# Kernel tuning notes

Hardware: AMD Instinct MI355X
Metric: run time of the kernel (lower is better)

The kernel has to match this reference:

```python
import jax, jax.numpy as jnp
import numpy as np

B = 8192
D = 626
TEMP = 0.25
EPS = 1e-8


def setup_inputs() -> dict:
    key = jax.random.key(0)
    k1, k2 = jax.random.split(key)
    anchors = jax.random.normal(k1, (B, D), dtype=jnp.float32)
    poss = jax.random.normal(k2, (B, D), dtype=jnp.float32)
    return {"anchors": anchors, "poss": poss}


def reference(anchors, poss):
    # Full pairwise cosine similarity: S[i, j] = cos(anchors[i], poss[j]).
    # torch.nn.CosineSimilarity: dot(x, y) / max(||x|| * ||y||, eps)
    na = jnp.linalg.norm(anchors, axis=1)          # [B]
    np_ = jnp.linalg.norm(poss, axis=1)            # [B]
    dots = anchors @ poss.T                        # [B, B]
    S = dots / jnp.maximum(na[:, None] * np_[None, :], EPS)

    diag = jnp.diagonal(S)                         # [B] positive-pair cosines
    logits = S / TEMP
    # loss_i = -log( exp(logits_ii) / sum_j exp(logits_ij) )
    loss = jax.nn.logsumexp(logits, axis=1) - jnp.diagonal(logits)

    n = S.shape[0]
    cos_an_pos = diag.mean()
    cos_an_neg = ((S.sum(axis=1) - diag) / (n - 1)).mean()
    return (loss.mean(), cos_an_pos, cos_an_neg)
```

## Files before the change

### kernel.cpp

```cpp
#include <hip/hip_runtime.h>
#include <stdint.h>

#define B_N   8192
#define D_K   626
#define KPAD  640
#define BK    128
#define KSTEPS 5
#define BM    128
#define BN    128
#define COL_CHUNKS 16
#define TILES_PER_CHUNK 4
#define FIN_BLOCKS 16

typedef __attribute__((ext_vector_type(4))) float f32x4;
typedef __attribute__((ext_vector_type(4))) int   i32x4;
typedef __attribute__((ext_vector_type(8))) int   i32x8;
typedef __attribute__((ext_vector_type(16))) float f32x16;

__device__ __forceinline__ void async16(const unsigned char* g, unsigned char* l) {
    __builtin_amdgcn_global_load_lds(
        (const __attribute__((address_space(1))) unsigned int*)(const void*)g,
        (__attribute__((address_space(3))) unsigned int*)(void*)l,
        16, 0, 0);
}

__global__ __launch_bounds__(256) void normalize_kernel(
    const float* __restrict__ A, const float* __restrict__ P,
    unsigned char* __restrict__ Af8, unsigned char* __restrict__ Pf8,
    float* __restrict__ rowexp, float* __restrict__ rowsum, float* __restrict__ acc)
{
    const int which = blockIdx.y;
    const float* srcM = which ? P : A;
    unsigned char* dstM = which ? Pf8 : Af8;
    const int t  = threadIdx.x;
    const int wv = t >> 6;
    const int L  = t & 63;
    const int rowBase = blockIdx.x * 8 + wv * 2;

    if (which == 0) {
        const int rb = blockIdx.x * 8;
        if (t < 8) { rowexp[rb + t] = 0.0f; rowsum[rb + t] = 0.0f; }
        if (blockIdx.x == 0 && t < 4) acc[t] = 0.0f;
    }

    #pragma unroll
    for (int j = 0; j < 2; ++j) {
        const int r = rowBase + j;
        const float2* s2 = (const float2*)(srcM + (size_t)r * D_K);

        float2 a0 = s2[2 * L];       float2 a1 = s2[2 * L + 1];
        float2 b0 = s2[2 * L + 128]; float2 b1 = s2[2 * L + 129];
        float2 c0 = {0.f, 0.f},      c1 = {0.f, 0.f};
        if (L < 28)       { c0 = s2[2 * L + 256]; c1 = s2[2 * L + 257]; }
        else if (L == 28) { c0 = s2[312]; }

        float ss = a0.x * a0.x + a0.y * a0.y + a1.x * a1.x + a1.y * a1.y
                 + b0.x * b0.x + b0.y * b0.y + b1.x * b1.x + b1.y * b1.y
                 + c0.x * c0.x + c0.y * c0.y + c1.x * c1.x + c1.y * c1.y;
        #pragma unroll
        for (int off = 32; off; off >>= 1) ss += __shfl_xor(ss, off, 64);
        const float rn = rsqrtf(ss);

        int* d4 = (int*)(dstM + (size_t)r * KPAD);
        int pk0 = __builtin_amdgcn_cvt_pk_fp8_f32(a0.x * rn, a0.y * rn, 0, false);
        pk0 = __builtin_amdgcn_cvt_pk_fp8_f32(a1.x * rn, a1.y * rn, pk0, true);
        d4[L] = pk0;
        int pk1 = __builtin_amdgcn_cvt_pk_fp8_f32(b0.x * rn, b0.y * rn, 0, false);
        pk1 = __builtin_amdgcn_cvt_pk_fp8_f32(b1.x * rn, b1.y * rn, pk1, true);
        d4[L + 64] = pk1;
        if (L < 32) {
            int pk2 = __builtin_amdgcn_cvt_pk_fp8_f32(c0.x * rn, c0.y * rn, 0, false);
            pk2 = __builtin_amdgcn_cvt_pk_fp8_f32(c1.x * rn, c1.y * rn, pk2, true);
            d4[L + 128] = pk2;
        }
    }
}

__global__ __launch_bounds__(256, 2) void gemm_fused_kernel(
    const unsigned char* __restrict__ Af8, const unsigned char* __restrict__ Pf8,
    float* __restrict__ rowexp, float* __restrict__ rowsum, float* __restrict__ diag)
{
    __shared__ __align__(16) unsigned char sA[2][BM * BK];
    __shared__ __align__(16) unsigned char sB[2][BN * BK];

    const int t    = threadIdx.x;
    const int lane = t & 63;
    const int w    = t >> 6;
    const int wr   = w >> 1;
    const int wc   = w & 1;
    const int rA   = lane & 31;
    const int h    = lane >> 5;
    const int rx   = rA & 7;

    const int rowBase = blockIdx.x * BM;
    const int chunk   = blockIdx.y;

    const int p0 = t, p1 = t + 256, p2 = t + 512, p3 = t + 768;
    const int r0 = p0 >> 3, r1 = p1 >> 3, r2 = p2 >> 3, r3 = p3 >> 3;
    const size_t g0 = (size_t)r0 * KPAD + (size_t)(((p0 & 7) ^ (r0 & 7)) * 16);
    const size_t g1 = (size_t)r1 * KPAD + (size_t)(((p1 & 7) ^ (r1 & 7)) * 16);
    const size_t g2 = (size_t)r2 * KPAD + (size_t)(((p2 & 7) ^ (r2 & 7)) * 16);
    const size_t g3 = (size_t)r3 * KPAD + (size_t)(((p3 & 7) ^ (r3 & 7)) * 16);

    const unsigned char* Ab = Af8 + (size_t)rowBase * KPAD;
    const unsigned char* PbChunk = Pf8 + (size_t)(chunk * TILES_PER_CHUNK) * BN * KPAD;

    float psum[2][16], pexp[2][16];
    #pragma unroll
    for (int i = 0; i < 2; ++i)
        #pragma unroll
        for (int j = 0; j < 16; ++j) { psum[i][j] = 0.0f; pexp[i][j] = 0.0f; }

    const f32x16 z16 = {0.f,0.f,0.f,0.f,0.f,0.f,0.f,0.f,
                        0.f,0.f,0.f,0.f,0.f,0.f,0.f,0.f};
    f32x16 acc[2][2];
    acc[0][0] = z16; acc[0][1] = z16; acc[1][0] = z16; acc[1][1] = z16;

    {
        async16(Ab + g0, &sA[0][p0 * 16]);
        async16(Ab + g1, &sA[0][p1 * 16]);
        async16(Ab + g2, &sA[0][p2 * 16]);
        async16(Ab + g3, &sA[0][p3 * 16]);
        async16(PbChunk + g0, &sB[0][p0 * 16]);
        async16(PbChunk + g1, &sB[0][p1 * 16]);
        async16(PbChunk + g2, &sB[0][p2 * 16]);
        async16(PbChunk + g3, &sB[0][p3 * 16]);
    }

    int par = 0;
    for (int ct = 0; ct < TILES_PER_CHUNK; ++ct) {
        #pragma unroll 1
        for (int ks = 0; ks < KSTEPS; ++ks) {
            __syncthreads();

            int nks = ks + 1, nct = ct;
            if (nks == KSTEPS) { nks = 0; ++nct; }
            if (nct < TILES_PER_CHUNK) {
                const int nxt = par ^ 1;
                const size_t nkOff = (size_t)nks * BK;
                const unsigned char* PbN = PbChunk + (size_t)nct * BN * KPAD + nkOff;
                const unsigned char* AbN = Ab + nkOff;
                async16(AbN + g0, &sA[nxt][p0 * 16]);
                async16(AbN + g1, &sA[nxt][p1 * 16]);
                async16(AbN + g2, &sA[nxt][p2 * 16]);
                async16(AbN + g3, &sA[nxt][p3 * 16]);
                async16(PbN + g0, &sB[nxt][p0 * 16]);
                async16(PbN + g1, &sB[nxt][p1 * 16]);
                async16(PbN + g2, &sB[nxt][p2 * 16]);
                async16(PbN + g3, &sB[nxt][p3 * 16]);
            }

            #pragma unroll
            for (int kb = 0; kb < 2; ++kb) {
                const int c0 = kb * 4 + 2 * h;
                const int s0 = ((c0    ) ^ rx) * 16;
                const int s1 = ((c0 + 1) ^ rx) * 16;

                i32x8 aF[2], bF[2];
                #pragma unroll
                for (int mi = 0; mi < 2; ++mi) {
                    const unsigned char* base = &sA[par][(wr * 64 + mi * 32 + rA) * BK];
                    i32x4 lo = *(const i32x4*)(base + s0);
                    i32x4 hi = *(const i32x4*)(base + s1);
                    aF[mi] = __builtin_shufflevector(lo, hi, 0, 1, 2, 3, 4, 5, 6, 7);
                }
                #pragma unroll
                for (int ni = 0; ni < 2; ++ni) {
                    const unsigned char* base = &sB[par][(wc * 64 + ni * 32 + rA) * BK];
                    i32x4 lo = *(const i32x4*)(base + s0);
                    i32x4 hi = *(const i32x4*)(base + s1);
                    bF[ni] = __builtin_shufflevector(lo, hi, 0, 1, 2, 3, 4, 5, 6, 7);
                }

                #pragma unroll
                for (int mi = 0; mi < 2; ++mi)
                    #pragma unroll
                    for (int ni = 0; ni < 2; ++ni)
                        acc[mi][ni] = __builtin_amdgcn_mfma_scale_f32_32x32x64_f8f6f4(
                            aF[mi], bF[ni], acc[mi][ni],
                            0 , 0 ,
                            0, 0x7F , 0, 0x7F );
            }
            par ^= 1;
        }

        const int colBase = (chunk * TILES_PER_CHUNK + ct) * BN;

        if (rowBase == colBase && wr == wc) {
            #pragma unroll
            for (int mi = 0; mi < 2; ++mi)
                #pragma unroll
                for (int rg = 0; rg < 16; ++rg) {
                    const int row32 = (rg & 3) + 8 * (rg >> 2) + 4 * h;
                    if (rA == row32)
                        diag[rowBase + wr * 64 + mi * 32 + row32] = acc[mi][mi][rg];
                }
        }

        #pragma unroll
        for (int mi = 0; mi < 2; ++mi) {
            #pragma unroll
            for (int rg = 0; rg < 16; ++rg) {
                const float S0 = acc[mi][0][rg];
                const float S1 = acc[mi][1][rg];
                psum[mi][rg] += S0 + S1;
                pexp[mi][rg] += __expf(S0 * 4.0f) + __expf(S1 * 4.0f);
            }
        }
        acc[0][0] = z16; acc[0][1] = z16; acc[1][0] = z16; acc[1][1] = z16;
    }

    #pragma unroll
    for (int off = 1; off <= 16; off <<= 1) {
        #pragma unroll
        for (int mi = 0; mi < 2; ++mi)
            #pragma unroll
            for (int rg = 0; rg < 16; ++rg) {
                psum[mi][rg] += __shfl_xor(psum[mi][rg], off, 64);
                pexp[mi][rg] += __shfl_xor(pexp[mi][rg], off, 64);
            }
    }
    if (rA == 0) {
        #pragma unroll
        for (int mi = 0; mi < 2; ++mi)
            #pragma unroll
            for (int rg = 0; rg < 16; ++rg) {
                const int gr = rowBase + wr * 64 + mi * 32
                             + (rg & 3) + 8 * (rg >> 2) + 4 * h;
                atomicAdd(&rowsum[gr], psum[mi][rg]);
                atomicAdd(&rowexp[gr], pexp[mi][rg]);
            }
    }
}

__global__ __launch_bounds__(256) void finalize_kernel(
    const float* __restrict__ rowexp, const float* __restrict__ rowsum,
    const float* __restrict__ diag, float* __restrict__ acc, float* __restrict__ out)
{
    const int t = threadIdx.x;
    float ls = 0.f, ds = 0.f, ns = 0.f;
    for (int i = blockIdx.x * 256 + t; i < B_N; i += FIN_BLOCKS * 256) {
        const float d = diag[i];
        ls += __logf(rowexp[i]) - d * 4.0f;
        ds += d;
        ns += (rowsum[i] - d);
    }
    #pragma unroll
    for (int off = 32; off; off >>= 1) {
        ls += __shfl_down(ls, off, 64);
        ds += __shfl_down(ds, off, 64);
        ns += __shfl_down(ns, off, 64);
    }
    __shared__ float sl[4], sd[4], sn[4];
    if ((t & 63) == 0) { sl[t >> 6] = ls; sd[t >> 6] = ds; sn[t >> 6] = ns; }
    __syncthreads();
    if (t == 0) {
        atomicAdd(acc + 0, sl[0] + sl[1] + sl[2] + sl[3]);
        atomicAdd(acc + 1, sd[0] + sd[1] + sd[2] + sd[3]);
        atomicAdd(acc + 2, sn[0] + sn[1] + sn[2] + sn[3]);
        __threadfence();
        const int done = (int)atomicAdd((unsigned int*)(acc + 3), 1u);
        if (done == FIN_BLOCKS - 1) {
            const float L  = atomicAdd(acc + 0, 0.0f);
            const float Dm = atomicAdd(acc + 1, 0.0f);
            const float Nn = atomicAdd(acc + 2, 0.0f);
            out[0] = L / (float)B_N;
            out[1] = Dm / (float)B_N;
            out[2] = (Nn / (float)(B_N - 1)) / (float)B_N;
        }
    }
}

__global__ __launch_bounds__(256) void fb_norm(
    const float* __restrict__ A, const float* __restrict__ P,
    float* __restrict__ rna, float* __restrict__ rnp, float* __restrict__ acc)
{
    const int r = blockIdx.x;
    const float* src = blockIdx.y ? P : A;
    const int t = threadIdx.x;
    float ss = 0.f;
    for (int k = t; k < D_K; k += 256) { float v = src[(size_t)r * D_K + k]; ss += v * v; }
    #pragma unroll
    for (int off = 32; off; off >>= 1) ss += __shfl_down(ss, off, 64);
    __shared__ float sred[4];
    if ((t & 63) == 0) sred[t >> 6] = ss;
    __syncthreads();
    if (t == 0) {
        const float rn = rsqrtf(sred[0] + sred[1] + sred[2] + sred[3]);
        (blockIdx.y ? rnp : rna)[r] = rn;
    }
    if (blockIdx.x == 0 && blockIdx.y == 0 && t < 3) acc[t] = 0.0f;
}

__global__ __launch_bounds__(256) void fb_main(
    const float* __restrict__ A, const float* __restrict__ P,
    const float* __restrict__ rna, const float* __restrict__ rnp,
    float* __restrict__ acc)
{
    __shared__ float sa[D_K];
    __shared__ float red[12];
    const int i = blockIdx.x;
    const int t = threadIdx.x;
    const float rn = rna[i];
    for (int k = t; k < D_K; k += 256) sa[k] = A[(size_t)i * D_K + k] * rn;
    __syncthreads();
    const int w = t >> 6, lane = t & 63;
    float we = 0.f, wsum = 0.f, wd = 0.f;
    for (int j = w; j < B_N; j += 4) {
        float dot = 0.f;
        const float* p = P + (size_t)j * D_K;
        for (int k = lane; k < D_K; k += 64) dot += sa[k] * p[k];
        #pragma unroll
        for (int off = 32; off; off >>= 1) dot += __shfl_xor(dot, off, 64);
        const float S = dot * rnp[j];
        we += __expf(S * 4.0f);
        wsum += S;
        if (j == i) wd = S;
    }
    if (lane == 0) { red[w] = we; red[4 + w] = wsum; red[8 + w] = wd; }
    __syncthreads();
    if (t == 0) {
        const float E  = red[0] + red[1] + red[2] + red[3];
        const float Sm = red[4] + red[5] + red[6] + red[7];
        const float Dd = red[8] + red[9] + red[10] + red[11];
        atomicAdd(acc + 0, __logf(E) - 4.0f * Dd);
        atomicAdd(acc + 1, Dd);
        atomicAdd(acc + 2, Sm - Dd);
    }
}

__global__ void fb_fin(const float* __restrict__ acc, float* __restrict__ out)
{
    out[0] = acc[0] / (float)B_N;
    out[1] = acc[1] / (float)B_N;
    out[2] = acc[2] / ((float)(B_N - 1) * (float)B_N);
}

extern "C" void kernel_launch(void* const* d_in, const int* in_sizes, int n_in,
                              void* d_out, int out_size, void* d_ws, size_t ws_size,
                              hipStream_t stream)
{
    const float* A = (const float*)d_in[0];
    const float* P = (const float*)d_in[1];
    float* out = (float*)d_out;
    char* ws = (char*)d_ws;

    const size_t AF8_OFF  = 0;
    const size_t PF8_OFF  = AF8_OFF + (size_t)B_N * KPAD;
    const size_t REXP_OFF = PF8_OFF + (size_t)B_N * KPAD;
    const size_t RSUM_OFF = REXP_OFF + (size_t)B_N * sizeof(float);
    const size_t DIAG_OFF = RSUM_OFF + (size_t)B_N * sizeof(float);
    const size_t ACC_OFF  = DIAG_OFF + (size_t)B_N * sizeof(float);
    const size_t MAIN_REQ = ACC_OFF + 16;

    if (ws_size >= MAIN_REQ) {
        unsigned char* Af8 = (unsigned char*)(ws + AF8_OFF);
        unsigned char* Pf8 = (unsigned char*)(ws + PF8_OFF);
        float* rowexp = (float*)(ws + REXP_OFF);
        float* rowsum = (float*)(ws + RSUM_OFF);
        float* diag   = (float*)(ws + DIAG_OFF);
        float* acc    = (float*)(ws + ACC_OFF);

        normalize_kernel<<<dim3(B_N / 8, 2), 256, 0, stream>>>(A, P, Af8, Pf8,
                                                               rowexp, rowsum, acc);
        gemm_fused_kernel<<<dim3(B_N / BM, COL_CHUNKS), 256, 0, stream>>>(
            Af8, Pf8, rowexp, rowsum, diag);
        finalize_kernel<<<FIN_BLOCKS, 256, 0, stream>>>(rowexp, rowsum, diag, acc, out);
    } else {
        float* rna = (float*)ws;
        float* rnp = rna + B_N;
        float* acc = rnp + B_N;
        fb_norm<<<dim3(B_N, 2), 256, 0, stream>>>(A, P, rna, rnp, acc);
        fb_main<<<B_N, 256, 0, stream>>>(A, P, rna, rnp, acc);
        fb_fin<<<1, 1, 0, stream>>>(acc, out);
    }
}
```

Baseline: 151.4 us.

## Restructure FP8 GEMM into 256x256 tiles with triple-buffered BK=64 pipeline

```diff
diff --git a/kernel.cpp b/kernel.cpp
--- a/kernel.cpp
+++ b/kernel.cpp
@@ -4,15 +4,11 @@
 #define B_N   8192
 #define D_K   626
 #define KPAD  640
-#define BK    128
-#define KSTEPS 5
-#define BM    128
-#define BN    128
-#define COL_CHUNKS 16
-#define TILES_PER_CHUNK 4
+#define BK64  64
+#define NT    10
+#define BMN   256
 #define FIN_BLOCKS 16
 
-typedef __attribute__((ext_vector_type(4))) float f32x4;
 typedef __attribute__((ext_vector_type(4))) int   i32x4;
 typedef __attribute__((ext_vector_type(8))) int   i32x8;
 typedef __attribute__((ext_vector_type(16))) float f32x16;
@@ -76,12 +72,12 @@
     }
 }
 
-__global__ __launch_bounds__(256, 2) void gemm_fused_kernel(
+__global__ __launch_bounds__(512, 2) void gemm_fused_kernel(
     const unsigned char* __restrict__ Af8, const unsigned char* __restrict__ Pf8,
     float* __restrict__ rowexp, float* __restrict__ rowsum, float* __restrict__ diag)
 {
-    __shared__ __align__(16) unsigned char sA[2][BM * BK];
-    __shared__ __align__(16) unsigned char sB[2][BN * BK];
+    __shared__ __align__(16) unsigned char sA[3][BMN * BK64];
+    __shared__ __align__(16) unsigned char sB[3][BMN * BK64];
 
     const int t    = threadIdx.x;
     const int lane = t & 63;
@@ -90,146 +86,125 @@
     const int wc   = w & 1;
     const int rA   = lane & 31;
     const int h    = lane >> 5;
-    const int rx   = rA & 7;
-
-    const int rowBase = blockIdx.x * BM;
-    const int chunk   = blockIdx.y;
-
-    const int p0 = t, p1 = t + 256, p2 = t + 512, p3 = t + 768;
-    const int r0 = p0 >> 3, r1 = p1 >> 3, r2 = p2 >> 3, r3 = p3 >> 3;
-    const size_t g0 = (size_t)r0 * KPAD + (size_t)(((p0 & 7) ^ (r0 & 7)) * 16);
-    const size_t g1 = (size_t)r1 * KPAD + (size_t)(((p1 & 7) ^ (r1 & 7)) * 16);
-    const size_t g2 = (size_t)r2 * KPAD + (size_t)(((p2 & 7) ^ (r2 & 7)) * 16);
-    const size_t g3 = (size_t)r3 * KPAD + (size_t)(((p3 & 7) ^ (r3 & 7)) * 16);
+    const int key  = (rA >> 1) & 3;
+
+    const int bid  = blockIdx.x;
+    const int swz  = (bid & 7) * 128 + (bid >> 3);
+    const int rowBase = (swz >> 5) * BMN;
+    const int colBase = (swz & 31) * BMN;
 
     const unsigned char* Ab = Af8 + (size_t)rowBase * KPAD;
-    const unsigned char* PbChunk = Pf8 + (size_t)(chunk * TILES_PER_CHUNK) * BN * KPAD;
-
-    float psum[2][16], pexp[2][16];
-    #pragma unroll
-    for (int i = 0; i < 2; ++i)
-        #pragma unroll
-        for (int j = 0; j < 16; ++j) { psum[i][j] = 0.0f; pexp[i][j] = 0.0f; }
-
+    const unsigned char* Pb = Pf8 + (size_t)colBase * KPAD;
+
+    const int q0 = t, q1 = t + 512;
+    const int r0 = q0 >> 2, r1 = q1 >> 2;
+    const size_t gsrc0 = (size_t)r0 * KPAD + (size_t)(((q0 & 3) ^ ((r0 >> 1) & 3)) * 16);
+    const size_t gsrc1 = (size_t)r1 * KPAD + (size_t)(((q1 & 3) ^ ((r1 >> 1) & 3)) * 16);
+
+    auto stage = [&](int buf, int kt) {
+        const size_t kOff = (size_t)kt * BK64;
+        async16(Ab + kOff + gsrc0, &sA[buf][q0 * 16]);
+        async16(Ab + kOff + gsrc1, &sA[buf][q1 * 16]);
+        async16(Pb + kOff + gsrc0, &sB[buf][q0 * 16]);
+        async16(Pb + kOff + gsrc1, &sB[buf][q1 * 16]);
+    };
+
+    const int s0 = ((2 * h)     ^ key) * 16;
+    const int s1 = ((2 * h + 1) ^ key) * 16;
+
+    f32x16 acc[2][4];
     const f32x16 z16 = {0.f,0.f,0.f,0.f,0.f,0.f,0.f,0.f,
                         0.f,0.f,0.f,0.f,0.f,0.f,0.f,0.f};
-    f32x16 acc[2][2];
-    acc[0][0] = z16; acc[0][1] = z16; acc[1][0] = z16; acc[1][1] = z16;
-
-    {
-        async16(Ab + g0, &sA[0][p0 * 16]);
-        async16(Ab + g1, &sA[0][p1 * 16]);
-        async16(Ab + g2, &sA[0][p2 * 16]);
-        async16(Ab + g3, &sA[0][p3 * 16]);
-        async16(PbChunk + g0, &sB[0][p0 * 16]);
-        async16(PbChunk + g1, &sB[0][p1 * 16]);
-        async16(PbChunk + g2, &sB[0][p2 * 16]);
-        async16(PbChunk + g3, &sB[0][p3 * 16]);
-    }
-
-    int par = 0;
-    for (int ct = 0; ct < TILES_PER_CHUNK; ++ct) {
-        #pragma unroll 1
-        for (int ks = 0; ks < KSTEPS; ++ks) {
-            __syncthreads();
-
-            int nks = ks + 1, nct = ct;
-            if (nks == KSTEPS) { nks = 0; ++nct; }
-            if (nct < TILES_PER_CHUNK) {
-                const int nxt = par ^ 1;
-                const size_t nkOff = (size_t)nks * BK;
-                const unsigned char* PbN = PbChunk + (size_t)nct * BN * KPAD + nkOff;
-                const unsigned char* AbN = Ab + nkOff;
-                async16(AbN + g0, &sA[nxt][p0 * 16]);
-                async16(AbN + g1, &sA[nxt][p1 * 16]);
-                async16(AbN + g2, &sA[nxt][p2 * 16]);
-                async16(AbN + g3, &sA[nxt][p3 * 16]);
-                async16(PbN + g0, &sB[nxt][p0 * 16]);
-                async16(PbN + g1, &sB[nxt][p1 * 16]);
-                async16(PbN + g2, &sB[nxt][p2 * 16]);
-                async16(PbN + g3, &sB[nxt][p3 * 16]);
-            }
-
-            #pragma unroll
-            for (int kb = 0; kb < 2; ++kb) {
-                const int c0 = kb * 4 + 2 * h;
-                const int s0 = ((c0    ) ^ rx) * 16;
-                const int s1 = ((c0 + 1) ^ rx) * 16;
-
-                i32x8 aF[2], bF[2];
-                #pragma unroll
-                for (int mi = 0; mi < 2; ++mi) {
-                    const unsigned char* base = &sA[par][(wr * 64 + mi * 32 + rA) * BK];
-                    i32x4 lo = *(const i32x4*)(base + s0);
-                    i32x4 hi = *(const i32x4*)(base + s1);
-                    aF[mi] = __builtin_shufflevector(lo, hi, 0, 1, 2, 3, 4, 5, 6, 7);
-                }
-                #pragma unroll
-                for (int ni = 0; ni < 2; ++ni) {
-                    const unsigned char* base = &sB[par][(wc * 64 + ni * 32 + rA) * BK];
-                    i32x4 lo = *(const i32x4*)(base + s0);
-                    i32x4 hi = *(const i32x4*)(base + s1);
-                    bF[ni] = __builtin_shufflevector(lo, hi, 0, 1, 2, 3, 4, 5, 6, 7);
-                }
-
-                #pragma unroll
-                for (int mi = 0; mi < 2; ++mi)
-                    #pragma unroll
-                    for (int ni = 0; ni < 2; ++ni)
-                        acc[mi][ni] = __builtin_amdgcn_mfma_scale_f32_32x32x64_f8f6f4(
-                            aF[mi], bF[ni], acc[mi][ni],
-                            0 , 0 ,
-                            0, 0x7F , 0, 0x7F );
-            }
-            par ^= 1;
-        }
-
-        const int colBase = (chunk * TILES_PER_CHUNK + ct) * BN;
-
-        if (rowBase == colBase && wr == wc) {
-            #pragma unroll
-            for (int mi = 0; mi < 2; ++mi)
-                #pragma unroll
-                for (int rg = 0; rg < 16; ++rg) {
-                    const int row32 = (rg & 3) + 8 * (rg >> 2) + 4 * h;
-                    if (rA == row32)
-                        diag[rowBase + wr * 64 + mi * 32 + row32] = acc[mi][mi][rg];
-                }
-        }
-
+    #pragma unroll
+    for (int mi = 0; mi < 2; ++mi)
+        #pragma unroll
+        for (int ni = 0; ni < 4; ++ni) acc[mi][ni] = z16;
+
+    auto compute = [&](int buf) {
+        i32x8 aF[2], bF[4];
         #pragma unroll
         for (int mi = 0; mi < 2; ++mi) {
-            #pragma unroll
-            for (int rg = 0; rg < 16; ++rg) {
-                const float S0 = acc[mi][0][rg];
-                const float S1 = acc[mi][1][rg];
-                psum[mi][rg] += S0 + S1;
-                pexp[mi][rg] += __expf(S0 * 4.0f) + __expf(S1 * 4.0f);
-            }
-        }
-        acc[0][0] = z16; acc[0][1] = z16; acc[1][0] = z16; acc[1][1] = z16;
-    }
-
-    #pragma unroll
-    for (int off = 1; off <= 16; off <<= 1) {
+            const unsigned char* base = &sA[buf][(wr * 64 + mi * 32 + rA) * BK64];
+            i32x4 lo = *(const i32x4*)(base + s0);
+            i32x4 hi = *(const i32x4*)(base + s1);
+            aF[mi] = __builtin_shufflevector(lo, hi, 0, 1, 2, 3, 4, 5, 6, 7);
+        }
+        #pragma unroll
+        for (int ni = 0; ni < 4; ++ni) {
+            const unsigned char* base = &sB[buf][(wc * 128 + ni * 32 + rA) * BK64];
+            i32x4 lo = *(const i32x4*)(base + s0);
+            i32x4 hi = *(const i32x4*)(base + s1);
+            bF[ni] = __builtin_shufflevector(lo, hi, 0, 1, 2, 3, 4, 5, 6, 7);
+        }
+        __builtin_amdgcn_s_setprio(1);
         #pragma unroll
         for (int mi = 0; mi < 2; ++mi)
             #pragma unroll
-            for (int rg = 0; rg < 16; ++rg) {
-                psum[mi][rg] += __shfl_xor(psum[mi][rg], off, 64);
-                pexp[mi][rg] += __shfl_xor(pexp[mi][rg], off, 64);
-            }
-    }
-    if (rA == 0) {
+            for (int ni = 0; ni < 4; ++ni)
+                acc[mi][ni] = __builtin_amdgcn_mfma_scale_f32_32x32x64_f8f6f4(
+                    aF[mi], bF[ni], acc[mi][ni],
+                    0 , 0 ,
+                    0, 0x7F , 0, 0x7F );
+        __builtin_amdgcn_s_setprio(0);
+    };
+
+    stage(0, 0);
+    stage(1, 1);
+
+    int cur = 0;
+    #pragma unroll 1
+    for (int kt = 0; kt < NT - 1; ++kt) {
+        asm volatile("s_waitcnt vmcnt(4)" ::: "memory");
+        __builtin_amdgcn_s_barrier();
+        if (kt < NT - 2) {
+            int sb = cur + 2; if (sb >= 3) sb -= 3;
+            stage(sb, kt + 2);
+        }
+        compute(cur);
+        ++cur; if (cur == 3) cur = 0;
+    }
+    asm volatile("s_waitcnt vmcnt(0)" ::: "memory");
+    __builtin_amdgcn_s_barrier();
+    compute(cur);
+
+    if (rowBase == colBase) {
         #pragma unroll
         for (int mi = 0; mi < 2; ++mi)
             #pragma unroll
-            for (int rg = 0; rg < 16; ++rg) {
+            for (int ni = 0; ni < 4; ++ni)
+                if (wr * 64 + mi * 32 == wc * 128 + ni * 32) {
+                    #pragma unroll
+                    for (int rg = 0; rg < 16; ++rg) {
+                        const int row32 = (rg & 3) + 8 * (rg >> 2) + 4 * h;
+                        if (rA == row32)
+                            diag[rowBase + wr * 64 + mi * 32 + row32] = acc[mi][ni][rg];
+                    }
+                }
+    }
+
+    #pragma unroll
+    for (int mi = 0; mi < 2; ++mi) {
+        #pragma unroll
+        for (int rg = 0; rg < 16; ++rg) {
+            float s = 0.f, e = 0.f;
+            #pragma unroll
+            for (int ni = 0; ni < 4; ++ni) {
+                const float S = acc[mi][ni][rg];
+                s += S;
+                e += __expf(S * 4.0f);
+            }
+            #pragma unroll
+            for (int off = 1; off <= 16; off <<= 1) {
+                s += __shfl_xor(s, off, 64);
+                e += __shfl_xor(e, off, 64);
+            }
+            if (rA == 0) {
                 const int gr = rowBase + wr * 64 + mi * 32
                              + (rg & 3) + 8 * (rg >> 2) + 4 * h;
-                atomicAdd(&rowsum[gr], psum[mi][rg]);
-                atomicAdd(&rowexp[gr], pexp[mi][rg]);
+                atomicAdd(&rowsum[gr], s);
+                atomicAdd(&rowexp[gr], e);
             }
+        }
     }
 }
 
@@ -363,7 +338,7 @@
 
         normalize_kernel<<<dim3(B_N / 8, 2), 256, 0, stream>>>(A, P, Af8, Pf8,
                                                                rowexp, rowsum, acc);
-        gemm_fused_kernel<<<dim3(B_N / BM, COL_CHUNKS), 256, 0, stream>>>(
+        gemm_fused_kernel<<<dim3((B_N / BMN) * (B_N / BMN)), 512, 0, stream>>>(
             Af8, Pf8, rowexp, rowsum, diag);
         finalize_kernel<<<FIN_BLOCKS, 256, 0, stream>>>(rowexp, rowsum, diag, acc, out);
     } else {
```

New measurement: 293.6 us. +94.0%, slower.

## Deepen GEMM pipeline to 4-stage BK=64 ring with explicit vmcnt waits

Applied to the files above, without the earlier changes.

```diff
diff --git a/kernel.cpp b/kernel.cpp
--- a/kernel.cpp
+++ b/kernel.cpp
@@ -4,15 +4,15 @@
 #define B_N   8192
 #define D_K   626
 #define KPAD  640
-#define BK    128
-#define KSTEPS 5
+#define BK    64
+#define KSTEPS_CT 10
 #define BM    128
 #define BN    128
 #define COL_CHUNKS 16
 #define TILES_PER_CHUNK 4
+#define NSTEPS 40
 #define FIN_BLOCKS 16
 
-typedef __attribute__((ext_vector_type(4))) float f32x4;
 typedef __attribute__((ext_vector_type(4))) int   i32x4;
 typedef __attribute__((ext_vector_type(8))) int   i32x8;
 typedef __attribute__((ext_vector_type(16))) float f32x16;
@@ -80,8 +80,8 @@
     const unsigned char* __restrict__ Af8, const unsigned char* __restrict__ Pf8,
     float* __restrict__ rowexp, float* __restrict__ rowsum, float* __restrict__ diag)
 {
-    __shared__ __align__(16) unsigned char sA[2][BM * BK];
-    __shared__ __align__(16) unsigned char sB[2][BN * BK];
+    __shared__ __align__(16) unsigned char sA[4][BM * BK];
+    __shared__ __align__(16) unsigned char sB[4][BN * BK];
 
     const int t    = threadIdx.x;
     const int lane = t & 63;
@@ -90,20 +90,32 @@
     const int wc   = w & 1;
     const int rA   = lane & 31;
     const int h    = lane >> 5;
-    const int rx   = rA & 7;
+    const int par4 = (rA & 1) * 4;
+    const int srA0 = wr * 32 + (rA >> 1);
+    const int srB0 = wc * 32 + (rA >> 1);
 
     const int rowBase = blockIdx.x * BM;
     const int chunk   = blockIdx.y;
 
-    const int p0 = t, p1 = t + 256, p2 = t + 512, p3 = t + 768;
-    const int r0 = p0 >> 3, r1 = p1 >> 3, r2 = p2 >> 3, r3 = p3 >> 3;
-    const size_t g0 = (size_t)r0 * KPAD + (size_t)(((p0 & 7) ^ (r0 & 7)) * 16);
-    const size_t g1 = (size_t)r1 * KPAD + (size_t)(((p1 & 7) ^ (r1 & 7)) * 16);
-    const size_t g2 = (size_t)r2 * KPAD + (size_t)(((p2 & 7) ^ (r2 & 7)) * 16);
-    const size_t g3 = (size_t)r3 * KPAD + (size_t)(((p3 & 7) ^ (r3 & 7)) * 16);
-
     const unsigned char* Ab = Af8 + (size_t)rowBase * KPAD;
     const unsigned char* PbChunk = Pf8 + (size_t)(chunk * TILES_PER_CHUNK) * BN * KPAD;
+
+    const int q0 = t, q1 = t + 256;
+    const int sr0 = q0 >> 3, p0s = q0 & 7;
+    const int sr1 = q1 >> 3, p1s = q1 & 7;
+    const int l0 = p0s ^ ((sr0 & 7) ^ ((sr0 >> 3) & 1));
+    const int l1 = p1s ^ ((sr1 & 7) ^ ((sr1 >> 3) & 1));
+    const int gA0 = (2 * sr0 + (l0 >> 2)) * KPAD + (l0 & 3) * 16;
+    const int gA1 = (2 * sr1 + (l1 >> 2)) * KPAD + (l1 & 3) * 16;
+
+    auto stage = [&](int buf, int ct, int ks) {
+        const unsigned char* AbT = Ab + ks * BK;
+        const unsigned char* PbT = PbChunk + (size_t)ct * BN * KPAD + ks * BK;
+        async16(AbT + gA0, &sA[buf][q0 * 16]);
+        async16(AbT + gA1, &sA[buf][q1 * 16]);
+        async16(PbT + gA0, &sB[buf][q0 * 16]);
+        async16(PbT + gA1, &sB[buf][q1 * 16]);
+    };
 
     float psum[2][16], pexp[2][16];
     #pragma unroll
@@ -116,76 +128,42 @@
     f32x16 acc[2][2];
     acc[0][0] = z16; acc[0][1] = z16; acc[1][0] = z16; acc[1][1] = z16;
 
-    {
-        async16(Ab + g0, &sA[0][p0 * 16]);
-        async16(Ab + g1, &sA[0][p1 * 16]);
-        async16(Ab + g2, &sA[0][p2 * 16]);
-        async16(Ab + g3, &sA[0][p3 * 16]);
-        async16(PbChunk + g0, &sB[0][p0 * 16]);
-        async16(PbChunk + g1, &sB[0][p1 * 16]);
-        async16(PbChunk + g2, &sB[0][p2 * 16]);
-        async16(PbChunk + g3, &sB[0][p3 * 16]);
-    }
-
-    int par = 0;
-    for (int ct = 0; ct < TILES_PER_CHUNK; ++ct) {
-        #pragma unroll 1
-        for (int ks = 0; ks < KSTEPS; ++ks) {
-            __syncthreads();
-
-            int nks = ks + 1, nct = ct;
-            if (nks == KSTEPS) { nks = 0; ++nct; }
-            if (nct < TILES_PER_CHUNK) {
-                const int nxt = par ^ 1;
-                const size_t nkOff = (size_t)nks * BK;
-                const unsigned char* PbN = PbChunk + (size_t)nct * BN * KPAD + nkOff;
-                const unsigned char* AbN = Ab + nkOff;
-                async16(AbN + g0, &sA[nxt][p0 * 16]);
-                async16(AbN + g1, &sA[nxt][p1 * 16]);
-                async16(AbN + g2, &sA[nxt][p2 * 16]);
-                async16(AbN + g3, &sA[nxt][p3 * 16]);
-                async16(PbN + g0, &sB[nxt][p0 * 16]);
-                async16(PbN + g1, &sB[nxt][p1 * 16]);
-                async16(PbN + g2, &sB[nxt][p2 * 16]);
-                async16(PbN + g3, &sB[nxt][p3 * 16]);
-            }
-
-            #pragma unroll
-            for (int kb = 0; kb < 2; ++kb) {
-                const int c0 = kb * 4 + 2 * h;
-                const int s0 = ((c0    ) ^ rx) * 16;
-                const int s1 = ((c0 + 1) ^ rx) * 16;
-
-                i32x8 aF[2], bF[2];
-                #pragma unroll
-                for (int mi = 0; mi < 2; ++mi) {
-                    const unsigned char* base = &sA[par][(wr * 64 + mi * 32 + rA) * BK];
-                    i32x4 lo = *(const i32x4*)(base + s0);
-                    i32x4 hi = *(const i32x4*)(base + s1);
-                    aF[mi] = __builtin_shufflevector(lo, hi, 0, 1, 2, 3, 4, 5, 6, 7);
-                }
-                #pragma unroll
-                for (int ni = 0; ni < 2; ++ni) {
-                    const unsigned char* base = &sB[par][(wc * 64 + ni * 32 + rA) * BK];
-                    i32x4 lo = *(const i32x4*)(base + s0);
-                    i32x4 hi = *(const i32x4*)(base + s1);
-                    bF[ni] = __builtin_shufflevector(lo, hi, 0, 1, 2, 3, 4, 5, 6, 7);
-                }
-
-                #pragma unroll
-                for (int mi = 0; mi < 2; ++mi)
-                    #pragma unroll
-                    for (int ni = 0; ni < 2; ++ni)
-                        acc[mi][ni] = __builtin_amdgcn_mfma_scale_f32_32x32x64_f8f6f4(
-                            aF[mi], bF[ni], acc[mi][ni],
-                            0 , 0 ,
-                            0, 0x7F , 0, 0x7F );
-            }
-            par ^= 1;
-        }
-
-        const int colBase = (chunk * TILES_PER_CHUNK + ct) * BN;
-
+    auto compute = [&](int buf) {
+        i32x8 aF[2], bF[2];
+        #pragma unroll
+        for (int mi = 0; mi < 2; ++mi) {
+            const int sr  = srA0 + mi * 16;
+            const int key = (sr & 7) ^ ((sr >> 3) & 1);
+            const int s0  = ((par4 + 2 * h) ^ key) * 16;
+            const unsigned char* base = &sA[buf][sr * 128];
+            i32x4 lo = *(const i32x4*)(base + s0);
+            i32x4 hi = *(const i32x4*)(base + (s0 ^ 16));
+            aF[mi] = __builtin_shufflevector(lo, hi, 0, 1, 2, 3, 4, 5, 6, 7);
+        }
+        #pragma unroll
+        for (int ni = 0; ni < 2; ++ni) {
+            const int sr  = srB0 + ni * 16;
+            const int key = (sr & 7) ^ ((sr >> 3) & 1);
+            const int s0  = ((par4 + 2 * h) ^ key) * 16;
+            const unsigned char* base = &sB[buf][sr * 128];
+            i32x4 lo = *(const i32x4*)(base + s0);
+            i32x4 hi = *(const i32x4*)(base + (s0 ^ 16));
+            bF[ni] = __builtin_shufflevector(lo, hi, 0, 1, 2, 3, 4, 5, 6, 7);
+        }
+        __builtin_amdgcn_s_setprio(1);
+        #pragma unroll
+        for (int mi = 0; mi < 2; ++mi)
+            #pragma unroll
+            for (int ni = 0; ni < 2; ++ni)
+                acc[mi][ni] = __builtin_amdgcn_mfma_scale_f32_32x32x64_f8f6f4(
+                    aF[mi], bF[ni], acc[mi][ni],
+                    0 , 0 ,
+                    0, 0x7F , 0, 0x7F );
+        __builtin_amdgcn_s_setprio(0);
+    };
+
+    auto epilogue = [&](int cct) {
+        const int colBase = (chunk * TILES_PER_CHUNK + cct) * BN;
         if (rowBase == colBase && wr == wc) {
             #pragma unroll
             for (int mi = 0; mi < 2; ++mi)
@@ -196,7 +174,6 @@
                         diag[rowBase + wr * 64 + mi * 32 + row32] = acc[mi][mi][rg];
                 }
         }
-
         #pragma unroll
         for (int mi = 0; mi < 2; ++mi) {
             #pragma unroll
@@ -208,6 +185,27 @@
             }
         }
         acc[0][0] = z16; acc[0][1] = z16; acc[1][0] = z16; acc[1][1] = z16;
+    };
+
+    stage(0, 0, 0);
+    stage(1, 0, 1);
+    stage(2, 0, 2);
+
+    int sct = 0, sks = 3;
+    int cct = 0, cks = 0;
+    #pragma unroll 1
+    for (int s = 0; s < NSTEPS; ++s) {
+        if (s < NSTEPS - 2)       asm volatile("s_waitcnt vmcnt(8)" ::: "memory");
+        else if (s == NSTEPS - 2) asm volatile("s_waitcnt vmcnt(4)" ::: "memory");
+        else                      asm volatile("s_waitcnt vmcnt(0)" ::: "memory");
+        __builtin_amdgcn_s_barrier();
+
+        if (s + 3 < NSTEPS) {
+            stage((s + 3) & 3, sct, sks);
+            if (++sks == KSTEPS_CT) { sks = 0; ++sct; }
+        }
+        compute(s & 3);
+        if (++cks == KSTEPS_CT) { cks = 0; epilogue(cct); ++cct; }
     }
 
     #pragma unroll
```

New measurement: 162.0 us. 1.07x slower.
